# Kernel tuning notes

Measured on AMD Instinct MI355X. Metric: run time of the kernel, lower is better.

## Reference

```python
import jax, jax.numpy as jnp
import numpy as np

B, S, D, H = 2, 2048, 1024, 16
HD = D // H  # head_dim = 64


def setup_inputs() -> dict:
    key = jax.random.key(0)
    ks = jax.random.split(key, 5)
    scale = 1.0 / np.sqrt(D)
    return {
        "x": jax.random.normal(ks[0], (B, S, D), jnp.float32),
        "Wq": jax.random.normal(ks[1], (D, D), jnp.float32) * scale,
        "Wk": jax.random.normal(ks[2], (D, D), jnp.float32) * scale,
        "Wv": jax.random.normal(ks[3], (D, D), jnp.float32) * scale,
        "Wo": jax.random.normal(ks[4], (D, D), jnp.float32) * scale,
        "bo": jnp.zeros((D,), jnp.float32),
    }


def reference(x, Wq, Wk, Wv, Wo, bo):
    b, s, d = x.shape
    # torch nn.Linear: y = x @ W.T  (W stored [d_out, d_in])
    q = (x @ Wq.T).reshape(b, s, H, HD).transpose(0, 2, 1, 3)  # [b,h,s,hd]
    k = (x @ Wk.T).reshape(b, s, H, HD).transpose(0, 2, 1, 3)
    v = (x @ Wv.T).reshape(b, s, H, HD).transpose(0, 2, 1, 3)
    scores = jnp.einsum("bhqd,bhkd->bhqk", q, k) / jnp.sqrt(jnp.float32(HD))
    causal = jnp.triu(jnp.ones((s, s), dtype=bool), k=1)
    scores = jnp.where(causal[None, None], -jnp.inf, scores)
    attn = jax.nn.softmax(scores, axis=-1)
    ctx = jnp.einsum("bhqk,bhkd->bhqd", attn, v)
    ctx = ctx.transpose(0, 2, 1, 3).reshape(b, s, d)
    return ctx @ Wo.T + bo
```

## Files before the change

### kernel.cpp

```cpp
#include <hip/hip_runtime.h>

#define B_  2
#define S_  2048
#define D_  1024
#define H_  16
#define HD_ 64
#define M_  4096

typedef __attribute__((ext_vector_type(8))) short  short8;
typedef __attribute__((ext_vector_type(4))) float  floatx4;

__device__ __forceinline__ unsigned short f2bf(float f) {
  unsigned int u = __float_as_uint(f);
  u = (u + 0x7fffu + ((u >> 16) & 1u)) >> 16;
  return (unsigned short)u;
}

__device__ __forceinline__ void gl_lds16(const short* g, short* l) {
  __builtin_amdgcn_global_load_lds(
      (const __attribute__((address_space(1))) unsigned int*)g,
      (__attribute__((address_space(3))) unsigned int*)l, 16, 0, 0);
}

__global__ __launch_bounds__(256) void cast_kernel(
    const float* __restrict__ x,  const float* __restrict__ wq,
    const float* __restrict__ wk, const float* __restrict__ wv,
    const float* __restrict__ wo,
    short* __restrict__ xb,  short* __restrict__ wqb, short* __restrict__ wkb,
    short* __restrict__ wvb, short* __restrict__ wob) {
  const float* src; short* dst; int n8;
  switch (blockIdx.y) {
    case 0:  src = x;  dst = xb;  n8 = (M_ * D_) / 8; break;
    case 1:  src = wq; dst = wqb; n8 = (D_ * D_) / 8; break;
    case 2:  src = wk; dst = wkb; n8 = (D_ * D_) / 8; break;
    case 3:  src = wv; dst = wvb; n8 = (D_ * D_) / 8; break;
    default: src = wo; dst = wob; n8 = (D_ * D_) / 8; break;
  }
  int i = blockIdx.x * 256 + threadIdx.x;
  if (i >= n8) return;
  float4 a = ((const float4*)src)[2 * i];
  float4 b = ((const float4*)src)[2 * i + 1];
  short8 o;
  o[0] = (short)f2bf(a.x); o[1] = (short)f2bf(a.y);
  o[2] = (short)f2bf(a.z); o[3] = (short)f2bf(a.w);
  o[4] = (short)f2bf(b.x); o[5] = (short)f2bf(b.y);
  o[6] = (short)f2bf(b.z); o[7] = (short)f2bf(b.w);
  ((short8*)dst)[i] = o;
}

__global__ __launch_bounds__(256) void gemm_qkv(
    const short* __restrict__ xb,  const short* __restrict__ wqb,
    const short* __restrict__ wkb, const short* __restrict__ wvb,
    short* __restrict__ qo, short* __restrict__ ko, short* __restrict__ vto) {
  __shared__ alignas(16) short As[128 * 32];
  __shared__ alignas(16) short Bs[128 * 32];
  const int tid  = threadIdx.x;
  const int lane = tid & 63, wid = tid >> 6;
  const int quad = lane >> 4, l16 = lane & 15;
  const int bn = blockIdx.x, bm = blockIdx.y, z = blockIdx.z;
  const short* wsel = (z == 0) ? wqb : ((z == 1) ? wkb : wvb);
  const float scale = (z == 0) ? 0.125f * 1.44269504f : 1.0f;
  const int lrow = wid * 32 + (lane >> 2);
  const int lcol = (lane & 3) * 8;
  const short* ag0 = xb   + (bm * 128 + lrow) * D_ + lcol;
  const short* ag1 = ag0 + 16 * D_;
  const short* bg0 = wsel + (bn * 128 + lrow) * D_ + lcol;
  const short* bg1 = bg0 + 16 * D_;
  short* la0 = &As[(wid * 32) * 32];
  short* la1 = &As[(wid * 32 + 16) * 32];
  short* lb0 = &Bs[(wid * 32) * 32];
  short* lb1 = &Bs[(wid * 32 + 16) * 32];
  const int wm = (wid & 1) * 64, wn = (wid >> 1) * 64;
  floatx4 acc[4][4];
#pragma unroll
  for (int i = 0; i < 4; i++)
#pragma unroll
    for (int j = 0; j < 4; j++) acc[i][j] = (floatx4){0.f, 0.f, 0.f, 0.f};

  for (int k0 = 0; k0 < D_; k0 += 32) {
    __syncthreads();
    gl_lds16(ag0 + k0, la0);
    gl_lds16(ag1 + k0, la1);
    gl_lds16(bg0 + k0, lb0);
    gl_lds16(bg1 + k0, lb1);
    __syncthreads();
    short8 af[4], bf[4];
#pragma unroll
    for (int t = 0; t < 4; t++) af[t] = *(const short8*)&As[(wm + t * 16 + l16) * 32 + quad * 8];
#pragma unroll
    for (int t = 0; t < 4; t++) bf[t] = *(const short8*)&Bs[(wn + t * 16 + l16) * 32 + quad * 8];
#pragma unroll
    for (int tm = 0; tm < 4; tm++)
#pragma unroll
      for (int tn = 0; tn < 4; tn++)
        acc[tm][tn] = __builtin_amdgcn_mfma_f32_16x16x32_bf16(af[tm], bf[tn], acc[tm][tn], 0, 0, 0);
  }
#pragma unroll
  for (int tm = 0; tm < 4; tm++) {
#pragma unroll
    for (int tn = 0; tn < 4; tn++) {
      int n = bn * 128 + wn + tn * 16 + l16;
      int h = n >> 6, hd = n & 63;
#pragma unroll
      for (int r = 0; r < 4; r++) {
        int m = bm * 128 + wm + tm * 16 + quad * 4 + r;
        int b = m >> 11, s = m & 2047;
        unsigned short val = f2bf(acc[tm][tn][r] * scale);
        if (z == 2)
          vto[((b * H_ + h) * HD_ + hd) * S_ + s] = (short)val;
        else if (z == 1)
          ko[((b * H_ + h) * S_ + s) * HD_ + hd] = (short)val;
        else
          qo[((b * H_ + h) * S_ + s) * HD_ + hd] = (short)val;
      }
    }
  }
}

__global__ __launch_bounds__(256) void gemm_out(
    const short* __restrict__ cx, const short* __restrict__ wob,
    const float* __restrict__ bo, float* __restrict__ out) {
  __shared__ alignas(16) short As[128 * 32];
  __shared__ alignas(16) short Bs[64 * 32];
  const int tid  = threadIdx.x;
  const int lane = tid & 63, wid = tid >> 6;
  const int quad = lane >> 4, l16 = lane & 15;
  const int bn = blockIdx.x, bm = blockIdx.y;
  const int lrow = wid * 32 + (lane >> 2);
  const int lcol = (lane & 3) * 8;
  const short* ag0 = cx  + (bm * 128 + lrow) * D_ + lcol;
  const short* ag1 = ag0 + 16 * D_;
  const short* bg0 = wob + (bn * 64 + wid * 16 + (lane >> 2)) * D_ + lcol;
  short* la0 = &As[(wid * 32) * 32];
  short* la1 = &As[(wid * 32 + 16) * 32];
  short* lb0 = &Bs[(wid * 16) * 32];
  const int wm = (wid & 1) * 64, wn = (wid >> 1) * 32;
  floatx4 acc[4][2];
#pragma unroll
  for (int i = 0; i < 4; i++)
#pragma unroll
    for (int j = 0; j < 2; j++) acc[i][j] = (floatx4){0.f, 0.f, 0.f, 0.f};

  for (int k0 = 0; k0 < D_; k0 += 32) {
    __syncthreads();
    gl_lds16(ag0 + k0, la0);
    gl_lds16(ag1 + k0, la1);
    gl_lds16(bg0 + k0, lb0);
    __syncthreads();
    short8 af[4], bf[2];
#pragma unroll
    for (int t = 0; t < 4; t++) af[t] = *(const short8*)&As[(wm + t * 16 + l16) * 32 + quad * 8];
#pragma unroll
    for (int t = 0; t < 2; t++) bf[t] = *(const short8*)&Bs[(wn + t * 16 + l16) * 32 + quad * 8];
#pragma unroll
    for (int tm = 0; tm < 4; tm++)
#pragma unroll
      for (int tn = 0; tn < 2; tn++)
        acc[tm][tn] = __builtin_amdgcn_mfma_f32_16x16x32_bf16(af[tm], bf[tn], acc[tm][tn], 0, 0, 0);
  }
#pragma unroll
  for (int tn = 0; tn < 2; tn++) {
    int n = bn * 64 + wn + tn * 16 + l16;
    float bias = bo[n];
#pragma unroll
    for (int tm = 0; tm < 4; tm++) {
#pragma unroll
      for (int r = 0; r < 4; r++) {
        int m = bm * 128 + wm + tm * 16 + quad * 4 + r;
        out[m * D_ + n] = acc[tm][tn][r] + bias;
      }
    }
  }
}

__global__ __launch_bounds__(512) void attn_kernel(
    const short* __restrict__ qbuf, const short* __restrict__ kbuf,
    const short* __restrict__ vtbuf, short* __restrict__ ctx) {
  __shared__ alignas(16) short Ks[2][64][64];
  __shared__ alignas(16) short Vs[2][64][64];
  __shared__ alignas(16) short Ps[8][16][64];
  const int tid  = threadIdx.x;
  const int lane = tid & 63, wid = tid >> 6;
  const int quad = lane >> 4, l16 = lane & 15;
  const int bx = blockIdx.x, by = blockIdx.y;
  const int qt = ((by >> 4) & 1) ? bx : (15 - bx);
  const int bh = by;
  const int base = bh * (S_ * HD_);
  const int q0 = qt * 128 + wid * 16;
  const int NT = 2 * qt + 2;

  short8 qf0 = *(const short8*)(qbuf + base + (q0 + l16) * HD_ + quad * 8);
  short8 qf1 = *(const short8*)(qbuf + base + (q0 + l16) * HD_ + 32 + quad * 8);

  float lsum[4];
  floatx4 o[4];
#pragma unroll
  for (int r = 0; r < 4; r++) lsum[r] = 0.f;
#pragma unroll
  for (int nt = 0; nt < 4; nt++) o[nt] = (floatx4){0.f, 0.f, 0.f, 0.f};

  const int srow  = tid >> 3;
  const int sslot = tid & 7;
  const int swz   = ((sslot ^ (srow & 7)) << 3);
  const short* kg = kbuf  + base + srow * HD_ + sslot * 8;
  const short* vg = vtbuf + base + srow * S_  + sslot * 8;

  short8 kreg = *(const short8*)(kg);
  short8 vreg = *(const short8*)(vg);
  *(short8*)&Ks[0][srow][swz] = kreg;
  *(short8*)&Vs[0][srow][swz] = vreg;
  kreg = *(const short8*)(kg + 64 * HD_);
  vreg = *(const short8*)(vg + 64);
  __syncthreads();

  const int x16 = l16 & 7;
  for (int kt = 0; kt < NT; kt++) {
    const int b = kt & 1;
    if (kt + 1 < NT) {
      *(short8*)&Ks[b ^ 1][srow][swz] = kreg;
      *(short8*)&Vs[b ^ 1][srow][swz] = vreg;
    }
    if (kt + 2 < NT) {
      kreg = *(const short8*)(kg + (kt + 2) * 64 * HD_);
      vreg = *(const short8*)(vg + (kt + 2) * 64);
    }
    if (kt * 64 <= q0 + 15) {
      floatx4 sc[4];
      __builtin_amdgcn_s_setprio(1);
#pragma unroll
      for (int ct = 0; ct < 4; ct++) {
        int row = ct * 16 + l16, rx = row & 7;
        short8 kb0 = *(const short8*)&Ks[b][row][(quad ^ rx) << 3];
        short8 kb1 = *(const short8*)&Ks[b][row][((4 + quad) ^ rx) << 3];
        floatx4 zz = (floatx4){-32.f, -32.f, -32.f, -32.f};
        zz     = __builtin_amdgcn_mfma_f32_16x16x32_bf16(qf0, kb0, zz, 0, 0, 0);
        sc[ct] = __builtin_amdgcn_mfma_f32_16x16x32_bf16(qf1, kb1, zz, 0, 0, 0);
      }
      __builtin_amdgcn_s_setprio(0);
      if (kt * 64 + 63 > q0) {
#pragma unroll
        for (int ct = 0; ct < 4; ct++)
#pragma unroll
          for (int r = 0; r < 4; r++)
            if (kt * 64 + ct * 16 + l16 > q0 + quad * 4 + r) sc[ct][r] = -INFINITY;
      }
#pragma unroll
      for (int r = 0; r < 4; r++) {
        int prow = quad * 4 + r, px = prow & 7;
#pragma unroll
        for (int ct = 0; ct < 4; ct++) {
          float p = __builtin_amdgcn_exp2f(sc[ct][r]);
          lsum[r] += p;
          int cslot = ct * 2 + (l16 >> 3);
          Ps[wid][prow][((cslot ^ px) << 3) + x16] = (short)(__float_as_uint(p) >> 16);
        }
      }
      __builtin_amdgcn_s_setprio(1);
#pragma unroll
      for (int ks = 0; ks < 2; ks++) {
        short8 pa = *(const short8*)&Ps[wid][l16][((ks * 4 + quad) ^ x16) << 3];
#pragma unroll
        for (int nt = 0; nt < 4; nt++) {
          int vrow = nt * 16 + l16;
          short8 vb = *(const short8*)&Vs[b][vrow][((ks * 4 + quad) ^ (vrow & 7)) << 3];
          o[nt] = __builtin_amdgcn_mfma_f32_16x16x32_bf16(pa, vb, o[nt], 0, 0, 0);
        }
      }
      __builtin_amdgcn_s_setprio(0);
    }
    __syncthreads();
  }
#pragma unroll
  for (int r = 0; r < 4; r++) {
    float ls = lsum[r];
    ls += __shfl_xor(ls, 1);
    ls += __shfl_xor(ls, 2);
    ls += __shfl_xor(ls, 4);
    ls += __shfl_xor(ls, 8);
    float linv = 1.f / ls;
    int s = q0 + quad * 4 + r;
    int rowbase = ((bh >> 4) * S_ + s) * D_ + (bh & 15) * HD_;
#pragma unroll
    for (int nt = 0; nt < 4; nt++)
      ctx[rowbase + nt * 16 + l16] = (short)f2bf(o[nt][r] * linv);
  }
}

extern "C" void kernel_launch(void* const* d_in, const int* in_sizes, int n_in,
                              void* d_out, int out_size, void* d_ws, size_t ws_size,
                              hipStream_t stream) {
  const float* x  = (const float*)d_in[0];
  const float* wq = (const float*)d_in[1];
  const float* wk = (const float*)d_in[2];
  const float* wv = (const float*)d_in[3];
  const float* wo = (const float*)d_in[4];
  const float* bo = (const float*)d_in[5];
  float* out = (float*)d_out;

  char* ws = (char*)d_ws;
  short* xb  = (short*)(ws);
  short* wqb = (short*)(ws + (8u  << 20));
  short* wkb = (short*)(ws + (10u << 20));
  short* wvb = (short*)(ws + (12u << 20));
  short* wob = (short*)(ws + (14u << 20));
  short* qb  = (short*)(ws + (16u << 20));
  short* kb  = (short*)(ws + (24u << 20));
  short* cx  = (short*)(ws + (32u << 20));
  short* vtb = (short*)(ws + (40u << 20));

  cast_kernel<<<dim3(2048, 5), 256, 0, stream>>>(x, wq, wk, wv, wo, xb, wqb, wkb, wvb, wob);
  gemm_qkv   <<<dim3(8, 32, 3), 256, 0, stream>>>(xb, wqb, wkb, wvb, qb, kb, vtb);
  attn_kernel<<<dim3(16, 32),   512, 0, stream>>>(qb, kb, vtb, cx);
  gemm_out   <<<dim3(16, 32),   256, 0, stream>>>(cx, wob, bo, out);
}
```

Measured before the change: 177.5 us.

## Double K-tile depth in QKV GEMM and XOR-swizzle LDS layout

The QKV projection GEMM now stages a 64-wide K slice per iteration instead of 32, halving the number of barrier pairs per output tile. The LDS layout is XOR-swizzled by row on the 16-byte column chunk, applied both at the global-to-LDS load and at the fragment reads, to avoid bank conflicts on the row-major tiles. LDS usage doubles to 32 KB per block, which may lower occupancy, and there is still no double buffering.

```diff
diff --git a/kernel.cpp b/kernel.cpp
--- a/kernel.cpp
+++ b/kernel.cpp
@@ -52,24 +52,20 @@
     const short* __restrict__ xb,  const short* __restrict__ wqb,
     const short* __restrict__ wkb, const short* __restrict__ wvb,
     short* __restrict__ qo, short* __restrict__ ko, short* __restrict__ vto) {
-  __shared__ alignas(16) short As[128 * 32];
-  __shared__ alignas(16) short Bs[128 * 32];
+  __shared__ alignas(16) short As[128 * 64];
+  __shared__ alignas(16) short Bs[128 * 64];
   const int tid  = threadIdx.x;
   const int lane = tid & 63, wid = tid >> 6;
   const int quad = lane >> 4, l16 = lane & 15;
   const int bn = blockIdx.x, bm = blockIdx.y, z = blockIdx.z;
   const short* wsel = (z == 0) ? wqb : ((z == 1) ? wkb : wvb);
   const float scale = (z == 0) ? 0.125f * 1.44269504f : 1.0f;
-  const int lrow = wid * 32 + (lane >> 2);
-  const int lcol = (lane & 3) * 8;
-  const short* ag0 = xb   + (bm * 128 + lrow) * D_ + lcol;
-  const short* ag1 = ag0 + 16 * D_;
-  const short* bg0 = wsel + (bn * 128 + lrow) * D_ + lcol;
-  const short* bg1 = bg0 + 16 * D_;
-  short* la0 = &As[(wid * 32) * 32];
-  short* la1 = &As[(wid * 32 + 16) * 32];
-  short* lb0 = &Bs[(wid * 32) * 32];
-  short* lb1 = &Bs[(wid * 32 + 16) * 32];
+  const int lrow = lane >> 3;
+  const int gcol = ((lane & 7) ^ lrow) * 8;
+  const short* agA = xb   + (bm * 128 + wid * 8 + lrow) * D_ + gcol;
+  const short* agB = wsel + (bn * 128 + wid * 8 + lrow) * D_ + gcol;
+  short* lA = &As[(wid * 8) * 64];
+  short* lB = &Bs[(wid * 8) * 64];
   const int wm = (wid & 1) * 64, wn = (wid >> 1) * 64;
   floatx4 acc[4][4];
 #pragma unroll
@@ -77,23 +73,28 @@
 #pragma unroll
     for (int j = 0; j < 4; j++) acc[i][j] = (floatx4){0.f, 0.f, 0.f, 0.f};
 
-  for (int k0 = 0; k0 < D_; k0 += 32) {
-    __syncthreads();
-    gl_lds16(ag0 + k0, la0);
-    gl_lds16(ag1 + k0, la1);
-    gl_lds16(bg0 + k0, lb0);
-    gl_lds16(bg1 + k0, lb1);
-    __syncthreads();
-    short8 af[4], bf[4];
-#pragma unroll
-    for (int t = 0; t < 4; t++) af[t] = *(const short8*)&As[(wm + t * 16 + l16) * 32 + quad * 8];
-#pragma unroll
-    for (int t = 0; t < 4; t++) bf[t] = *(const short8*)&Bs[(wn + t * 16 + l16) * 32 + quad * 8];
-#pragma unroll
-    for (int tm = 0; tm < 4; tm++)
-#pragma unroll
-      for (int tn = 0; tn < 4; tn++)
-        acc[tm][tn] = __builtin_amdgcn_mfma_f32_16x16x32_bf16(af[tm], bf[tn], acc[tm][tn], 0, 0, 0);
+  for (int k0 = 0; k0 < D_; k0 += 64) {
+    __syncthreads();
+#pragma unroll
+    for (int c = 0; c < 4; c++) {
+      gl_lds16(agA + c * 32 * D_ + k0, lA + c * 32 * 64);
+      gl_lds16(agB + c * 32 * D_ + k0, lB + c * 32 * 64);
+    }
+    __syncthreads();
+#pragma unroll
+    for (int kk = 0; kk < 2; kk++) {
+      const int sx = ((kk * 4 + quad) ^ (l16 & 7)) * 8;
+      short8 af[4], bf[4];
+#pragma unroll
+      for (int t = 0; t < 4; t++) af[t] = *(const short8*)&As[(wm + t * 16 + l16) * 64 + sx];
+#pragma unroll
+      for (int t = 0; t < 4; t++) bf[t] = *(const short8*)&Bs[(wn + t * 16 + l16) * 64 + sx];
+#pragma unroll
+      for (int tm = 0; tm < 4; tm++)
+#pragma unroll
+        for (int tn = 0; tn < 4; tn++)
+          acc[tm][tn] = __builtin_amdgcn_mfma_f32_16x16x32_bf16(af[tm], bf[tn], acc[tm][tn], 0, 0, 0);
+    }
   }
 #pragma unroll
   for (int tm = 0; tm < 4; tm++) {
```

Result: slower. 192.1 us (+8.2%).

## Double-buffer LDS tiles in QKV GEMM to overlap loads with MFMA

Applied to the files above, without the earlier changes.

Double-buffers the QKV projection GEMM's shared-memory tiles. The next K-slice is issued via global_load_lds into the alternate buffer while MFMAs run on the current one, with one barrier per iteration instead of two. This aims to hide global-load latency behind compute, at the cost of twice the LDS footprint. That could lower occupancy, and it relies on explicit waitcnt/barrier ordering for correctness.

```diff
diff --git a/kernel.cpp b/kernel.cpp
--- a/kernel.cpp
+++ b/kernel.cpp
@@ -52,8 +52,8 @@
     const short* __restrict__ xb,  const short* __restrict__ wqb,
     const short* __restrict__ wkb, const short* __restrict__ wvb,
     short* __restrict__ qo, short* __restrict__ ko, short* __restrict__ vto) {
-  __shared__ alignas(16) short As[128 * 32];
-  __shared__ alignas(16) short Bs[128 * 32];
+  __shared__ alignas(16) short As[2][128 * 32];
+  __shared__ alignas(16) short Bs[2][128 * 32];
   const int tid  = threadIdx.x;
   const int lane = tid & 63, wid = tid >> 6;
   const int quad = lane >> 4, l16 = lane & 15;
@@ -66,10 +66,12 @@
   const short* ag1 = ag0 + 16 * D_;
   const short* bg0 = wsel + (bn * 128 + lrow) * D_ + lcol;
   const short* bg1 = bg0 + 16 * D_;
-  short* la0 = &As[(wid * 32) * 32];
-  short* la1 = &As[(wid * 32 + 16) * 32];
-  short* lb0 = &Bs[(wid * 32) * 32];
-  short* lb1 = &Bs[(wid * 32 + 16) * 32];
+  short* la0 = &As[0][(wid * 32) * 32];
+  short* la1 = &As[0][(wid * 32 + 16) * 32];
+  short* lb0 = &Bs[0][(wid * 32) * 32];
+  short* lb1 = &Bs[0][(wid * 32 + 16) * 32];
+  const short* As0 = &As[0][0];
+  const short* Bs0 = &Bs[0][0];
   const int wm = (wid & 1) * 64, wn = (wid >> 1) * 64;
   floatx4 acc[4][4];
 #pragma unroll
@@ -77,24 +79,39 @@
 #pragma unroll
     for (int j = 0; j < 4; j++) acc[i][j] = (floatx4){0.f, 0.f, 0.f, 0.f};
 
-  for (int k0 = 0; k0 < D_; k0 += 32) {
-    __syncthreads();
-    gl_lds16(ag0 + k0, la0);
-    gl_lds16(ag1 + k0, la1);
-    gl_lds16(bg0 + k0, lb0);
-    gl_lds16(bg1 + k0, lb1);
-    __syncthreads();
+  gl_lds16(ag0, la0);
+  gl_lds16(ag1, la1);
+  gl_lds16(bg0, lb0);
+  gl_lds16(bg1, lb1);
+  asm volatile("s_waitcnt vmcnt(0)" ::: "memory");
+  __builtin_amdgcn_s_barrier();
+
+  int cur = 0;
+  for (int t = 0; t < 32; ++t) {
+    if (t + 1 < 32) {
+      const int k1 = (t + 1) * 32;
+      const int off = (cur ^ 1) * (128 * 32);
+      gl_lds16(ag0 + k1, la0 + off);
+      gl_lds16(ag1 + k1, la1 + off);
+      gl_lds16(bg0 + k1, lb0 + off);
+      gl_lds16(bg1 + k1, lb1 + off);
+    }
+    const int rb = cur * (128 * 32);
     short8 af[4], bf[4];
 #pragma unroll
-    for (int t = 0; t < 4; t++) af[t] = *(const short8*)&As[(wm + t * 16 + l16) * 32 + quad * 8];
-#pragma unroll
-    for (int t = 0; t < 4; t++) bf[t] = *(const short8*)&Bs[(wn + t * 16 + l16) * 32 + quad * 8];
+    for (int i = 0; i < 4; i++) af[i] = *(const short8*)&As0[rb + (wm + i * 16 + l16) * 32 + quad * 8];
+#pragma unroll
+    for (int i = 0; i < 4; i++) bf[i] = *(const short8*)&Bs0[rb + (wn + i * 16 + l16) * 32 + quad * 8];
 #pragma unroll
     for (int tm = 0; tm < 4; tm++)
 #pragma unroll
       for (int tn = 0; tn < 4; tn++)
         acc[tm][tn] = __builtin_amdgcn_mfma_f32_16x16x32_bf16(af[tm], bf[tn], acc[tm][tn], 0, 0, 0);
-  }
+    asm volatile("s_waitcnt vmcnt(0)" ::: "memory");
+    __builtin_amdgcn_s_barrier();
+    cur ^= 1;
+  }
+
 #pragma unroll
   for (int tm = 0; tm < 4; tm++) {
 #pragma unroll
```

After: 183.4 us. +3.3%, slower.
